# Performance work log

Hardware: AMD Instinct MI355X
Metric: run time of the kernel (lower is better)

The kernel has to match this reference:

```python
import jax, jax.numpy as jnp
import numpy as np
from jax import lax

DN = ('NCHW', 'OIHW', 'NCHW')

def conv(x, w, b, stride, pad):
    y = lax.conv_general_dilated(x, w, (stride, stride), [(pad, pad), (pad, pad)], dimension_numbers=DN)
    return y + b[None, :, None, None]

def setup_inputs() -> dict:
    key = jax.random.key(0)
    ks = jax.random.split(key, 16)
    s = 0.05
    inp = {
        'condition': jax.random.normal(ks[0], (16, 1, 256, 256), jnp.float32),
        'w1': jax.random.normal(ks[1], (64, 1, 4, 4), jnp.float32) * s,
        'b1': jnp.zeros((64,), jnp.float32),
        'w2': jax.random.normal(ks[2], (128, 64, 4, 4), jnp.float32) * s,
        'b2': jnp.zeros((128,), jnp.float32),
        'w3': jax.random.normal(ks[3], (128, 128, 3, 3), jnp.float32) * s,
        'b3': jnp.zeros((128,), jnp.float32),
        'r1w1': jax.random.normal(ks[4], (32, 128, 3, 3), jnp.float32) * s,
        'r1b1': jnp.zeros((32,), jnp.float32),
        'r1w2': jax.random.normal(ks[5], (128, 32, 1, 1), jnp.float32) * s,
        'r1b2': jnp.zeros((128,), jnp.float32),
        'r2w1': jax.random.normal(ks[6], (32, 128, 3, 3), jnp.float32) * s,
        'r2b1': jnp.zeros((32,), jnp.float32),
        'r2w2': jax.random.normal(ks[7], (128, 32, 1, 1), jnp.float32) * s,
        'r2b2': jnp.zeros((128,), jnp.float32),
        'wpre': jax.random.normal(ks[8], (4, 128, 1, 1), jnp.float32) * s,
        'bpre': jnp.zeros((4,), jnp.float32),
        'codebook': jax.random.normal(ks[9], (2048, 4), jnp.float32),
    }
    return inp

def reference(condition, w1, b1, w2, b2, w3, b3, r1w1, r1b1, r1w2, r1b2,
              r2w1, r2b1, r2w2, r2b2, wpre, bpre, codebook):
    # --- conv encoder (VQ-VAE standard) ---
    h = jax.nn.relu(conv(condition, w1, b1, 2, 1))   # [B,64,128,128]
    h = jax.nn.relu(conv(h, w2, b2, 2, 1))           # [B,128,64,64]
    h = conv(h, w3, b3, 1, 1)                        # [B,128,64,64]
    # residual stack: 2 blocks of relu->3x3->relu->1x1, residual add
    for wa, ba, wb, bb in ((r1w1, r1b1, r1w2, r1b2), (r2w1, r2b1, r2w2, r2b2)):
        t = conv(jax.nn.relu(h), wa, ba, 1, 1)
        t = conv(jax.nn.relu(t), wb, bb, 1, 0)
        h = h + t
    h = jax.nn.relu(h)
    z = conv(h, wpre, bpre, 1, 0)                    # [B,4,64,64]
    # --- cosine-distance vector quantization ---
    B, D, H, W = z.shape
    zf = jnp.transpose(z, (0, 2, 3, 1)).reshape(-1, D)          # [BHW, D]
    zn = zf / (jnp.linalg.norm(zf, axis=-1, keepdims=True) + 1e-12)
    en = codebook / (jnp.linalg.norm(codebook, axis=-1, keepdims=True) + 1e-12)
    sim = jnp.einsum('nd,kd->nk', zn, en)                       # cosine similarity
    idx = jnp.argmax(sim, axis=-1)                              # nearest code
    q = codebook[idx].reshape(B, H, W, D)
    c = jnp.transpose(q, (0, 3, 1, 2))                          # [B,4,64,64]
    return c
```

## Files before the change

kernel.cpp:

```cpp
#include <hip/hip_runtime.h>
#include <math.h>


typedef short v8s __attribute__((ext_vector_type(8)));
typedef float v4f __attribute__((ext_vector_type(4)));

#define B_OFF 4194304
#define A_OFF 12582912
#define W2_S 0
#define W3_S 393216
#define WR1_S 835584
#define WR2_S 946176
#define WP1_S 1056768
#define WP2_S 1069056

__device__ inline void limb3(float v, unsigned short& h, unsigned short& m,
                             unsigned short& l) {
    unsigned ub = __float_as_uint(v);
    unsigned hb = ub & 0xffff0000u;
    float r1 = v - __uint_as_float(hb);
    unsigned mb = __float_as_uint(r1) & 0xffff0000u;
    float r2 = r1 - __uint_as_float(mb);
    unsigned lb = __float_as_uint(r2) & 0xffff0000u;
    h = (unsigned short)(hb >> 16);
    m = (unsigned short)(mb >> 16);
    l = (unsigned short)(lb >> 16);
}

struct CfgConv2 {
    static constexpr int NC = 8, NT = 4, OC = 128, ICG = 64, IN_H = 128, IN_W = 128;
    static constexpr bool RELU_IN = false, RELU_OUT = true;
    __device__ static void tap(int c, int t, int& ry, int& rx) {
        int py = (c >> 2) & 1, px = (c >> 1) & 1;
        ry = (t >> 1) - py; rx = (t & 1) - px;
    }
    __device__ static void inaddr(int c, int oy, int r, int X,
                                  int& Yg, int& Xg, int& ic0) {
        int py = (c >> 2) & 1, px = (c >> 1) & 1;
        Yg = 2 * (oy + r - 1) + py; Xg = 2 * X + px; ic0 = (c & 1) * 32;
    }
    __device__ static int widx(int c, int t, int oc, int ic) {
        int py = (c >> 2) & 1, px = (c >> 1) & 1, half = c & 1;
        int dy = 2 * (t >> 1) + (1 - py), dx = 2 * (t & 1) + (1 - px);
        return ((oc * 64 + half * 32 + ic) * 4 + dy) * 4 + dx;
    }
};
struct CfgConv3 {
    static constexpr int NC = 4, NT = 9, OC = 128, ICG = 128, IN_H = 64, IN_W = 64;
    static constexpr bool RELU_IN = false, RELU_OUT = false;
    __device__ static void tap(int c, int t, int& ry, int& rx) {
        ry = t / 3 - 1; rx = t % 3 - 1;
    }
    __device__ static void inaddr(int c, int oy, int r, int X,
                                  int& Yg, int& Xg, int& ic0) {
        Yg = oy + r - 1; Xg = X; ic0 = c * 32;
    }
    __device__ static int widx(int c, int t, int oc, int ic) {
        return ((oc * 128 + c * 32 + ic) * 3 + t / 3) * 3 + t % 3;
    }
};
struct CfgRes {
    static constexpr int NC = 4, NT = 9, OC = 32, ICG = 128, IN_H = 64, IN_W = 64;
    __device__ static int widx(int c, int t, int oc, int ic) {
        return ((oc * 128 + c * 32 + ic) * 3 + t / 3) * 3 + t % 3;
    }
};
struct Cfg1x1 {
    static constexpr int NC = 1, NT = 1, OC = 128;
    __device__ static int widx(int c, int t, int oc, int ic) {
        return oc * 32 + ic;
    }
};

template <typename C>
__device__ inline void repack_one(const float* __restrict__ w,
                                  short* __restrict__ dst, int idx) {
    int s  = idx & 31;
    int oc = (idx >> 5) % C::OC;
    int ct = idx / (32 * C::OC);
    int c = ct / C::NT, t = ct % C::NT;
    float val = w[C::widx(c, t, oc, s)];
    unsigned short h, m, l;
    limb3(val, h, m, l);
    constexpr int NTILE = C::OC / 16;
    int nt = oc >> 4, o = oc & 15, q = s >> 3, j = s & 7;
    int fr = ((q * 16 + o) << 3) + j;
    dst[(((ct * 3 + 0) * NTILE + nt) << 9) + fr] = (short)h;
    dst[(((ct * 3 + 1) * NTILE + nt) << 9) + fr] = (short)m;
    dst[(((ct * 3 + 2) * NTILE + nt) << 9) + fr] = (short)l;
}

__global__ __launch_bounds__(256) void repack_all_k(
    const float* __restrict__ w2, const float* __restrict__ w3,
    const float* __restrict__ r1, const float* __restrict__ r2,
    const float* __restrict__ p1, const float* __restrict__ p2,
    short* __restrict__ base)
{
    int idx = blockIdx.x * 256 + threadIdx.x;
    if (idx < 131072) { repack_one<CfgConv2>(w2, base + W2_S, idx); return; }
    idx -= 131072;
    if (idx < 147456) { repack_one<CfgConv3>(w3, base + W3_S, idx); return; }
    idx -= 147456;
    if (idx < 36864)  { repack_one<CfgRes>(r1, base + WR1_S, idx); return; }
    idx -= 36864;
    if (idx < 36864)  { repack_one<CfgRes>(r2, base + WR2_S, idx); return; }
    idx -= 36864;
    if (idx < 4096)   { repack_one<Cfg1x1>(p1, base + WP1_S, idx); return; }
    idx -= 4096;
    if (idx < 4096)   { repack_one<Cfg1x1>(p2, base + WP2_S, idx); }
}

template <typename C>
__global__ __launch_bounds__(256, 3) void mfma_conv(
    const float* __restrict__ in, const short* __restrict__ repw,
    const float* __restrict__ bias, float* __restrict__ out, int n0)
{
    constexpr int APLANE = 3 * 66 * 32;
    constexpr int NTILE  = C::OC / 16;
    __shared__ __align__(16) short lA[3 * APLANE];

    int tid = threadIdx.x;
    int lane = tid & 63, wv = tid >> 6;
    int n_img = blockIdx.x >> 6, oy = blockIdx.x & 63;

    for (int idx = tid; idx < 3 * 3 * 2 * 16; idx += 256) {
        int plane = idx / 96;
        int rem = idx % 96;
        int rr = rem / 32;
        int hc = (rem / 16) & 1;
        int d = idx & 15;
        ((unsigned*)lA)[plane * 3168 + (rr * 66 + hc * 65) * 16 + d] = 0;
    }

    v4f acc[4][2] = {};
    int nbase = wv * 2;
    int Xq = tid & 15, icp = tid >> 4, quad = lane >> 4;

    float pv[24];
    auto issue_loads = [&](int c) {
#pragma unroll
        for (int it = 0; it < 12; it++) {
            int r = it >> 2, xg = it & 3;
            int X = xg * 16 + Xq;
            int Yg, Xg, ic0;
            C::inaddr(c, oy, r, X, Yg, Xg, ic0);
            float v0 = 0.f, v1 = 0.f;
            if (Yg >= 0 && Yg < C::IN_H) {
                int g = ((n_img * C::ICG + ic0 + 2 * icp) * C::IN_H + Yg) * C::IN_W + Xg;
                v0 = in[g];
                v1 = in[g + C::IN_H * C::IN_W];
            }
            pv[2 * it] = v0; pv[2 * it + 1] = v1;
        }
    };
    auto load_bf = [&](int c, int t, v8s (&dst)[2][3]) {
#pragma unroll
        for (int nt = 0; nt < 2; nt++)
#pragma unroll
            for (int L = 0; L < 3; L++)
                dst[nt][L] = *(const v8s*)(repw +
                    ((((c * C::NT + t) * 3 + L) * NTILE + (nbase + nt)) << 9) +
                    (lane << 3));
    };

    issue_loads(0);

    for (int c = 0; c < C::NC; c++) {
        __syncthreads();
#pragma unroll
        for (int it = 0; it < 12; it++) {
            int r = it >> 2, xg = it & 3;
            int X = xg * 16 + Xq;
            float v0 = pv[2 * it], v1 = pv[2 * it + 1];
            if constexpr (C::RELU_IN) { v0 = fmaxf(v0, 0.f); v1 = fmaxf(v1, 0.f); }
            unsigned short h0, m0, l0, h1, m1, l1;
            limb3(v0, h0, m0, l0);
            limb3(v1, h1, m1, l1);
            int cell = r * 66 + X + 1;
            int f = (cell + (cell >> 2)) & 3;
            int phys = (icp & 3) + 4 * (((icp >> 2) + f) & 3);
            unsigned* pa = (unsigned*)lA + cell * 16 + phys;
            pa[0]        = (unsigned)h0 | ((unsigned)h1 << 16);
            pa[3168]     = (unsigned)m0 | ((unsigned)m1 << 16);
            pa[2 * 3168] = (unsigned)l0 | ((unsigned)l1 << 16);
        }
        __syncthreads();
        if (c + 1 < C::NC) issue_loads(c + 1);

        v8s bf[2][2][3];
        load_bf(c, 0, bf[0]);
#pragma unroll
        for (int t = 0; t < C::NT; t++) {
            constexpr int NTT = C::NT;
            if (t + 1 < NTT) load_bf(c, t + 1, bf[(t + 1) & 1]);
            int ry, rx;
            C::tap(c, t, ry, rx);
#pragma unroll
            for (int mt = 0; mt < 4; mt++) {
                int x = mt * 16 + (lane & 15);
                int cell = (ry + 1) * 66 + (x + rx + 1);
                int f = (cell + (cell >> 2)) & 3;
                int aa = cell * 32 + (((quad + f) & 3) << 3);
                v8s ah = *(const v8s*)&lA[aa];
                v8s am = *(const v8s*)&lA[APLANE + aa];
                v8s al = *(const v8s*)&lA[2 * APLANE + aa];
#pragma unroll
                for (int nt = 0; nt < 2; nt++) {
                    v4f a0 = acc[mt][nt];
                    a0 = __builtin_amdgcn_mfma_f32_16x16x32_bf16(ah, bf[t & 1][nt][0], a0, 0, 0, 0);
                    a0 = __builtin_amdgcn_mfma_f32_16x16x32_bf16(ah, bf[t & 1][nt][1], a0, 0, 0, 0);
                    a0 = __builtin_amdgcn_mfma_f32_16x16x32_bf16(am, bf[t & 1][nt][0], a0, 0, 0, 0);
                    a0 = __builtin_amdgcn_mfma_f32_16x16x32_bf16(am, bf[t & 1][nt][1], a0, 0, 0, 0);
                    a0 = __builtin_amdgcn_mfma_f32_16x16x32_bf16(ah, bf[t & 1][nt][2], a0, 0, 0, 0);
                    a0 = __builtin_amdgcn_mfma_f32_16x16x32_bf16(al, bf[t & 1][nt][0], a0, 0, 0, 0);
                    acc[mt][nt] = a0;
                }
            }
        }
    }
#pragma unroll
    for (int mt = 0; mt < 4; mt++) {
        int x0 = mt * 16 + quad * 4;
#pragma unroll
        for (int nt = 0; nt < 2; nt++) {
            int oc = (nbase + nt) * 16 + (lane & 15);
            float bv = bias[oc];
            float v0 = acc[mt][nt][0] + bv;
            float v1 = acc[mt][nt][1] + bv;
            float v2 = acc[mt][nt][2] + bv;
            float v3 = acc[mt][nt][3] + bv;
            if constexpr (C::RELU_OUT) {
                v0 = fmaxf(v0, 0.f); v1 = fmaxf(v1, 0.f);
                v2 = fmaxf(v2, 0.f); v3 = fmaxf(v3, 0.f);
            }
            float4 o = make_float4(v0, v1, v2, v3);
            *(float4*)&out[(((n0 + n_img) * C::OC + oc) * 64 + oy) * 64 + x0] = o;
        }
    }
}

__global__ __launch_bounds__(256) void mfma_res(
    const float* __restrict__ in, const short* __restrict__ repw,
    const float* __restrict__ b1, const short* __restrict__ repp,
    const float* __restrict__ b2, float* __restrict__ out)
{
    constexpr int PLANE_D = 4 * 66 * 16;
    constexpr int PLANE_S = 2 * PLANE_D;
    __shared__ __align__(16) short lA[3 * PLANE_S];

    int tid = threadIdx.x;
    int lane = tid & 63, wv = tid >> 6;
    int n_img = blockIdx.x >> 5;
    int oy0 = (blockIdx.x & 31) << 1;
    int jrow = wv >> 1, xh = wv & 1;

    for (int idx = tid; idx < 3 * 4 * 2 * 16; idx += 256) {
        int plane = idx / 128;
        int rem = idx % 128;
        int rr = rem / 32;
        int hc = (rem >> 4) & 1;
        int d = idx & 15;
        ((unsigned*)lA)[plane * PLANE_D + (rr * 66 + hc * 65) * 16 + d] = 0;
    }

    v4f acc[2][2] = {};
    int Xq = tid & 15, icp = tid >> 4, quad = lane >> 4;

    float pv[32];
    auto issue_loads = [&](int c) {
#pragma unroll
        for (int it = 0; it < 16; it++) {
            int r = it >> 2, xg = it & 3;
            int X = xg * 16 + Xq;
            int Yg = oy0 + r - 1;
            float v0 = 0.f, v1 = 0.f;
            if (Yg >= 0 && Yg < 64) {
                int g = ((n_img * 128 + c * 32 + 2 * icp) * 64 + Yg) * 64 + X;
                v0 = in[g];
                v1 = in[g + 4096];
            }
            pv[2 * it] = v0; pv[2 * it + 1] = v1;
        }
    };

    issue_loads(0);

    for (int c = 0; c < 4; c++) {
        __syncthreads();
#pragma unroll
        for (int it = 0; it < 16; it++) {
            int r = it >> 2, xg = it & 3;
            int X = xg * 16 + Xq;
            float v0 = fmaxf(pv[2 * it], 0.f);
            float v1 = fmaxf(pv[2 * it + 1], 0.f);
            unsigned short h0, m0, l0, h1, m1, l1;
            limb3(v0, h0, m0, l0);
            limb3(v1, h1, m1, l1);
            int cell = r * 66 + X + 1;
            int f = (cell + (cell >> 2)) & 3;
            int phys = (icp & 3) + 4 * (((icp >> 2) + f) & 3);
            unsigned* pa = (unsigned*)lA + cell * 16 + phys;
            pa[0]           = (unsigned)h0 | ((unsigned)h1 << 16);
            pa[PLANE_D]     = (unsigned)m0 | ((unsigned)m1 << 16);
            pa[2 * PLANE_D] = (unsigned)l0 | ((unsigned)l1 << 16);
        }
        __syncthreads();
        if (c + 1 < 4) issue_loads(c + 1);

        v8s bf[2][2][3];
        auto load_bf = [&](int t, v8s (&dst)[2][3]) {
#pragma unroll
            for (int nt = 0; nt < 2; nt++)
#pragma unroll
                for (int L = 0; L < 3; L++)
                    dst[nt][L] = *(const v8s*)(repw +
                        ((((c * 9 + t) * 3 + L) * 2 + nt) << 9) + (lane << 3));
        };
        load_bf(0, bf[0]);
#pragma unroll
        for (int t = 0; t < 9; t++) {
            if (t + 1 < 9) load_bf(t + 1, bf[(t + 1) & 1]);
            int ry = t / 3 - 1, rx = t % 3 - 1;
#pragma unroll
            for (int mti = 0; mti < 2; mti++) {
                int x = (xh * 2 + mti) * 16 + (lane & 15);
                int cell = (jrow + ry + 1) * 66 + (x + rx + 1);
                int f = (cell + (cell >> 2)) & 3;
                int aa = cell * 32 + (((quad + f) & 3) << 3);
                v8s ah = *(const v8s*)&lA[aa];
                v8s am = *(const v8s*)&lA[PLANE_S + aa];
                v8s al = *(const v8s*)&lA[2 * PLANE_S + aa];
#pragma unroll
                for (int nt = 0; nt < 2; nt++) {
                    v4f a0 = acc[mti][nt];
                    a0 = __builtin_amdgcn_mfma_f32_16x16x32_bf16(ah, bf[t & 1][nt][0], a0, 0, 0, 0);
                    a0 = __builtin_amdgcn_mfma_f32_16x16x32_bf16(ah, bf[t & 1][nt][1], a0, 0, 0, 0);
                    a0 = __builtin_amdgcn_mfma_f32_16x16x32_bf16(am, bf[t & 1][nt][0], a0, 0, 0, 0);
                    a0 = __builtin_amdgcn_mfma_f32_16x16x32_bf16(am, bf[t & 1][nt][1], a0, 0, 0, 0);
                    a0 = __builtin_amdgcn_mfma_f32_16x16x32_bf16(ah, bf[t & 1][nt][2], a0, 0, 0, 0);
                    a0 = __builtin_amdgcn_mfma_f32_16x16x32_bf16(al, bf[t & 1][nt][0], a0, 0, 0, 0);
                    acc[mti][nt] = a0;
                }
            }
        }
    }

    __syncthreads();
#pragma unroll
    for (int mti = 0; mti < 2; mti++) {
#pragma unroll
        for (int nt = 0; nt < 2; nt++) {
            int ic = nt * 16 + (lane & 15);
            int icp2 = ic >> 1, hilo = ic & 1;
            float bv = b1[ic];
#pragma unroll
            for (int r = 0; r < 4; r++) {
                int x = (xh * 2 + mti) * 16 + quad * 4 + r;
                float v = fmaxf(acc[mti][nt][r] + bv, 0.f);
                unsigned short h, m, l;
                limb3(v, h, m, l);
                int f = (x + (x >> 2)) & 3;
                int phys = (icp2 & 3) + 4 * (((icp2 >> 2) + f) & 3);
                int sa = x * 32 + phys * 2 + hilo;
                lA[jrow * 6144 + sa]        = (short)h;
                lA[jrow * 6144 + 2048 + sa] = (short)m;
                lA[jrow * 6144 + 4096 + sa] = (short)l;
            }
        }
    }
    __syncthreads();

#pragma unroll
    for (int j = 0; j < 2; j++) {
        v4f a2[8] = {};
        int x = wv * 16 + (lane & 15);
        int f = (x + (x >> 2)) & 3;
        int aa = x * 32 + (((quad + f) & 3) << 3);
        v8s ah = *(const v8s*)&lA[j * 6144 + aa];
        v8s am = *(const v8s*)&lA[j * 6144 + 2048 + aa];
        v8s al = *(const v8s*)&lA[j * 6144 + 4096 + aa];
#pragma unroll
        for (int nt = 0; nt < 8; nt++) {
            v8s bh = *(const v8s*)(repp + ((0 * 8 + nt) << 9) + (lane << 3));
            v8s bm = *(const v8s*)(repp + ((1 * 8 + nt) << 9) + (lane << 3));
            v8s bl = *(const v8s*)(repp + ((2 * 8 + nt) << 9) + (lane << 3));
            v4f a0 = a2[nt];
            a0 = __builtin_amdgcn_mfma_f32_16x16x32_bf16(ah, bh, a0, 0, 0, 0);
            a0 = __builtin_amdgcn_mfma_f32_16x16x32_bf16(ah, bm, a0, 0, 0, 0);
            a0 = __builtin_amdgcn_mfma_f32_16x16x32_bf16(am, bh, a0, 0, 0, 0);
            a0 = __builtin_amdgcn_mfma_f32_16x16x32_bf16(am, bm, a0, 0, 0, 0);
            a0 = __builtin_amdgcn_mfma_f32_16x16x32_bf16(ah, bl, a0, 0, 0, 0);
            a0 = __builtin_amdgcn_mfma_f32_16x16x32_bf16(al, bh, a0, 0, 0, 0);
            a2[nt] = a0;
        }
#pragma unroll
        for (int nt = 0; nt < 8; nt++) {
            int oc = nt * 16 + (lane & 15);
            int x0 = wv * 16 + quad * 4;
            int off = ((n_img * 128 + oc) * 64 + (oy0 + j)) * 64 + x0;
            float4 hv = *(const float4*)&in[off];
            float bv = b2[oc];
            float4 o = make_float4(hv.x + a2[nt][0] + bv, hv.y + a2[nt][1] + bv,
                                   hv.z + a2[nt][2] + bv, hv.w + a2[nt][3] + bv);
            *(float4*)&out[off] = o;
        }
    }
}

__global__ __launch_bounds__(256) void conv1_k(
    const float* __restrict__ x, const float* __restrict__ w,
    const float* __restrict__ b, float* __restrict__ out)
{
    int tid = blockIdx.x * 256 + threadIdx.x;
    int n   = tid >> 14;
    int rem = tid & 16383;
    int oy  = rem >> 7;
    int ox  = rem & 127;
    int iy0 = oy * 2 - 1, ix0 = ox * 2 - 1;
    const float* xb = x + n * 65536;
    float v[16];
#pragma unroll
    for (int ky = 0; ky < 4; ky++) {
#pragma unroll
        for (int kx = 0; kx < 4; kx++) {
            int iy = iy0 + ky, ix = ix0 + kx;
            bool ok = (iy >= 0) & (iy < 256) & (ix >= 0) & (ix < 256);
            v[ky * 4 + kx] = ok ? xb[iy * 256 + ix] : 0.f;
        }
    }
    int obase = (n * 64) * 16384 + (oy << 7) + ox;
    for (int oc = 0; oc < 64; oc++) {
        float acc = b[oc];
        const float* wp = w + oc * 16;
#pragma unroll
        for (int k = 0; k < 16; k++) acc = fmaf(v[k], wp[k], acc);
        out[obase + oc * 16384] = fmaxf(acc, 0.f);
    }
}

__global__ __launch_bounds__(256) void prevq_k(
    const float* __restrict__ h, const float* __restrict__ wpre,
    const float* __restrict__ bpre, const float* __restrict__ cb,
    float* __restrict__ out)
{
    __shared__ float4 en[2048];
    for (int i = threadIdx.x; i < 2048; i += 256) {
        float c0 = cb[i * 4 + 0], c1 = cb[i * 4 + 1];
        float c2 = cb[i * 4 + 2], c3 = cb[i * 4 + 3];
        float nrm = sqrtf(c0 * c0 + c1 * c1 + c2 * c2 + c3 * c3) + 1e-12f;
        en[i] = make_float4(c0 / nrm, c1 / nrm, c2 / nrm, c3 / nrm);
    }
    __syncthreads();

    int tid = blockIdx.x * 256 + threadIdx.x;
    int n   = tid >> 12;
    int pos = tid & 4095;
    const float* hb = h + n * 128 * 4096 + pos;
    float z0 = bpre[0], z1 = bpre[1], z2 = bpre[2], z3 = bpre[3];
    for (int ic = 0; ic < 128; ic++) {
        float v = fmaxf(hb[ic * 4096], 0.f);
        z0 = fmaf(v, wpre[ic],       z0);
        z1 = fmaf(v, wpre[128 + ic], z1);
        z2 = fmaf(v, wpre[256 + ic], z2);
        z3 = fmaf(v, wpre[384 + ic], z3);
    }
    float best = -1e30f;
    int   bidx = 0;
    for (int k = 0; k < 2048; k++) {
        float4 e = en[k];
        float s = z0 * e.x + z1 * e.y + z2 * e.z + z3 * e.w;
        if (s > best) { best = s; bidx = k; }
    }
    const float* q = cb + bidx * 4;
    out[(n * 4 + 0) * 4096 + pos] = q[0];
    out[(n * 4 + 1) * 4096 + pos] = q[1];
    out[(n * 4 + 2) * 4096 + pos] = q[2];
    out[(n * 4 + 3) * 4096 + pos] = q[3];
}

extern "C" void kernel_launch(void* const* d_in, const int* in_sizes, int n_in,
                              void* d_out, int out_size, void* d_ws, size_t ws_size,
                              hipStream_t stream)
{
    const float* x    = (const float*)d_in[0];
    const float* w1   = (const float*)d_in[1];
    const float* b1   = (const float*)d_in[2];
    const float* w2   = (const float*)d_in[3];
    const float* b2   = (const float*)d_in[4];
    const float* w3   = (const float*)d_in[5];
    const float* b3   = (const float*)d_in[6];
    const float* r1w1 = (const float*)d_in[7];
    const float* r1b1 = (const float*)d_in[8];
    const float* r1w2 = (const float*)d_in[9];
    const float* r1b2 = (const float*)d_in[10];
    const float* r2w1 = (const float*)d_in[11];
    const float* r2b1 = (const float*)d_in[12];
    const float* r2w2 = (const float*)d_in[13];
    const float* r2b2 = (const float*)d_in[14];
    const float* wpre = (const float*)d_in[15];
    const float* bpre = (const float*)d_in[16];
    const float* cb   = (const float*)d_in[17];
    float* out = (float*)d_out;

    float* ws   = (float*)d_ws;
    short* wsS  = (short*)d_ws;
    float* B = ws + B_OFF;
    float* A = ws + A_OFF;

    repack_all_k<<<1408, 256, 0, stream>>>(w2, w3, r1w1, r2w1, r1w2, r2w2, wsS);

    conv1_k<<<512, 256, 0, stream>>>(x,               w1, b1, A);
    mfma_conv<CfgConv2><<<512, 256, 0, stream>>>(A, wsS + W2_S, b2, B, 0);
    conv1_k<<<512, 256, 0, stream>>>(x + 8 * 65536,   w1, b1, A);
    mfma_conv<CfgConv2><<<512, 256, 0, stream>>>(A, wsS + W2_S, b2, B, 8);

    mfma_conv<CfgConv3><<<1024, 256, 0, stream>>>(B, wsS + W3_S, b3, A, 0);

    mfma_res<<<512, 256, 0, stream>>>(A, wsS + WR1_S, r1b1, wsS + WP1_S, r1b2, B);
    mfma_res<<<512, 256, 0, stream>>>(B, wsS + WR2_S, r2b1, wsS + WP2_S, r2b2, A);

    prevq_k<<<256, 256, 0, stream>>>(A, wpre, bpre, cb, out);
}
```

Baseline: 480.4 us.

## Store intermediate activations in row-major channel-pair interleaved layout

```diff
diff --git a/kernel.cpp b/kernel.cpp
--- a/kernel.cpp
+++ b/kernel.cpp
@@ -28,16 +28,21 @@
 }
 
 struct CfgConv2 {
-    static constexpr int NC = 8, NT = 4, OC = 128, ICG = 64, IN_H = 128, IN_W = 128;
+    static constexpr int NC = 8, NT = 4, OC = 128;
     static constexpr bool RELU_IN = false, RELU_OUT = true;
     __device__ static void tap(int c, int t, int& ry, int& rx) {
         int py = (c >> 2) & 1, px = (c >> 1) & 1;
         ry = (t >> 1) - py; rx = (t & 1) - px;
     }
-    __device__ static void inaddr(int c, int oy, int r, int X,
-                                  int& Yg, int& Xg, int& ic0) {
+    __device__ static bool gaddr(int n, int oy, int r, int X, int icp, int c,
+                                 int& g0, int& g1) {
         int py = (c >> 2) & 1, px = (c >> 1) & 1;
-        Yg = 2 * (oy + r - 1) + py; Xg = 2 * X + px; ic0 = (c & 1) * 32;
+        int Yg = 2 * (oy + r - 1) + py;
+        if (Yg < 0 || Yg >= 128) return false;
+        int pi = (c & 1) * 16 + icp;
+        g0 = ((n * 128 + Yg) * 32 + pi) * 256 + 2 * X + px;
+        g1 = g0 + 128;
+        return true;
     }
     __device__ static int widx(int c, int t, int oc, int ic) {
         int py = (c >> 2) & 1, px = (c >> 1) & 1, half = c & 1;
@@ -46,21 +51,26 @@
     }
 };
 struct CfgConv3 {
-    static constexpr int NC = 4, NT = 9, OC = 128, ICG = 128, IN_H = 64, IN_W = 64;
+    static constexpr int NC = 4, NT = 9, OC = 128;
     static constexpr bool RELU_IN = false, RELU_OUT = false;
     __device__ static void tap(int c, int t, int& ry, int& rx) {
         ry = t / 3 - 1; rx = t % 3 - 1;
     }
-    __device__ static void inaddr(int c, int oy, int r, int X,
-                                  int& Yg, int& Xg, int& ic0) {
-        Yg = oy + r - 1; Xg = X; ic0 = c * 32;
+    __device__ static bool gaddr(int n, int oy, int r, int X, int icp, int c,
+                                 int& g0, int& g1) {
+        int Yg = oy + r - 1;
+        if (Yg < 0 || Yg >= 64) return false;
+        int pi = c * 16 + icp;
+        g0 = ((n * 64 + Yg) * 64 + pi) * 128 + X;
+        g1 = g0 + 64;
+        return true;
     }
     __device__ static int widx(int c, int t, int oc, int ic) {
         return ((oc * 128 + c * 32 + ic) * 3 + t / 3) * 3 + t % 3;
     }
 };
 struct CfgRes {
-    static constexpr int NC = 4, NT = 9, OC = 32, ICG = 128, IN_H = 64, IN_W = 64;
+    static constexpr int NC = 4, NT = 9, OC = 32;
     __device__ static int widx(int c, int t, int oc, int ic) {
         return ((oc * 128 + c * 32 + ic) * 3 + t / 3) * 3 + t % 3;
     }
@@ -142,13 +152,11 @@
         for (int it = 0; it < 12; it++) {
             int r = it >> 2, xg = it & 3;
             int X = xg * 16 + Xq;
-            int Yg, Xg, ic0;
-            C::inaddr(c, oy, r, X, Yg, Xg, ic0);
+            int g0, g1;
             float v0 = 0.f, v1 = 0.f;
-            if (Yg >= 0 && Yg < C::IN_H) {
-                int g = ((n_img * C::ICG + ic0 + 2 * icp) * C::IN_H + Yg) * C::IN_W + Xg;
-                v0 = in[g];
-                v1 = in[g + C::IN_H * C::IN_W];
+            if (C::gaddr(n_img, oy, r, X, icp, c, g0, g1)) {
+                v0 = in[g0];
+                v1 = in[g1];
             }
             pv[2 * it] = v0; pv[2 * it + 1] = v1;
         }
@@ -175,6 +183,7 @@
             if constexpr (C::RELU_IN) { v0 = fmaxf(v0, 0.f); v1 = fmaxf(v1, 0.f); }
             unsigned short h0, m0, l0, h1, m1, l1;
             limb3(v0, h0, m0, l0);
+            limb3(v1, m1, m1, l1);
             limb3(v1, h1, m1, l1);
             int cell = r * 66 + X + 1;
             int f = (cell + (cell >> 2)) & 3;
@@ -234,7 +243,9 @@
                 v2 = fmaxf(v2, 0.f); v3 = fmaxf(v3, 0.f);
             }
             float4 o = make_float4(v0, v1, v2, v3);
-            *(float4*)&out[(((n0 + n_img) * C::OC + oc) * 64 + oy) * 64 + x0] = o;
+            int off = (((n0 + n_img) * 64 + oy) * 64 + (oc >> 1)) * 128 +
+                      (oc & 1) * 64 + x0;
+            *(float4*)&out[off] = o;
         }
     }
 }
@@ -275,9 +286,9 @@
             int Yg = oy0 + r - 1;
             float v0 = 0.f, v1 = 0.f;
             if (Yg >= 0 && Yg < 64) {
-                int g = ((n_img * 128 + c * 32 + 2 * icp) * 64 + Yg) * 64 + X;
+                int g = ((n_img * 64 + Yg) * 64 + (c * 16 + icp)) * 128 + X;
                 v0 = in[g];
-                v1 = in[g + 4096];
+                v1 = in[g + 64];
             }
             pv[2 * it] = v0; pv[2 * it + 1] = v1;
         }
@@ -397,7 +408,8 @@
         for (int nt = 0; nt < 8; nt++) {
             int oc = nt * 16 + (lane & 15);
             int x0 = wv * 16 + quad * 4;
-            int off = ((n_img * 128 + oc) * 64 + (oy0 + j)) * 64 + x0;
+            int off = ((n_img * 64 + (oy0 + j)) * 64 + (oc >> 1)) * 128 +
+                      (oc & 1) * 64 + x0;
             float4 hv = *(const float4*)&in[off];
             float bv = b2[oc];
             float4 o = make_float4(hv.x + a2[nt][0] + bv, hv.y + a2[nt][1] + bv,
@@ -428,13 +440,13 @@
             v[ky * 4 + kx] = ok ? xb[iy * 256 + ix] : 0.f;
         }
     }
-    int obase = (n * 64) * 16384 + (oy << 7) + ox;
+    int obase = (n * 128 + oy) * 8192 + ox;
     for (int oc = 0; oc < 64; oc++) {
         float acc = b[oc];
         const float* wp = w + oc * 16;
 #pragma unroll
         for (int k = 0; k < 16; k++) acc = fmaf(v[k], wp[k], acc);
-        out[obase + oc * 16384] = fmaxf(acc, 0.f);
+        out[obase + (oc >> 1) * 256 + (oc & 1) * 128] = fmaxf(acc, 0.f);
     }
 }
 
@@ -455,14 +467,21 @@
     int tid = blockIdx.x * 256 + threadIdx.x;
     int n   = tid >> 12;
     int pos = tid & 4095;
-    const float* hb = h + n * 128 * 4096 + pos;
+    int y = pos >> 6, xx = pos & 63;
+    const float* hb = h + ((n * 64 + y) * 64) * 128 + xx;
     float z0 = bpre[0], z1 = bpre[1], z2 = bpre[2], z3 = bpre[3];
-    for (int ic = 0; ic < 128; ic++) {
-        float v = fmaxf(hb[ic * 4096], 0.f);
-        z0 = fmaf(v, wpre[ic],       z0);
-        z1 = fmaf(v, wpre[128 + ic], z1);
-        z2 = fmaf(v, wpre[256 + ic], z2);
-        z3 = fmaf(v, wpre[384 + ic], z3);
+    for (int icp = 0; icp < 64; icp++) {
+        float v0 = fmaxf(hb[icp * 128], 0.f);
+        int ic = 2 * icp;
+        z0 = fmaf(v0, wpre[ic],       z0);
+        z1 = fmaf(v0, wpre[128 + ic], z1);
+        z2 = fmaf(v0, wpre[256 + ic], z2);
+        z3 = fmaf(v0, wpre[384 + ic], z3);
+        float v1 = fmaxf(hb[icp * 128 + 64], 0.f);
+        z0 = fmaf(v1, wpre[ic + 1],       z0);
+        z1 = fmaf(v1, wpre[128 + ic + 1], z1);
+        z2 = fmaf(v1, wpre[256 + ic + 1], z2);
+        z3 = fmaf(v1, wpre[384 + ic + 1], z3);
     }
     float best = -1e30f;
     int   bidx = 0;
```

New measurement: 462.3 us. 3.8% less time.
